# Kernel tuning notes

Measured on AMD Instinct MI355X. Metric: run time of the kernel, lower is better.

Reference implementation:

```python
import jax, jax.numpy as jnp
import numpy as np

B, C_IN, C_OUT, L = 16, 512, 512, 2048
HEADS, K, U, KS, PAD = 4, 16, 1, 3, 1
VV = C_OUT // HEADS  # 128
EPS = 1e-5


def _conv1d(x, w, pad):
    # x: [B, Cin, L], w: [Cout, Cin, KS] -> [B, Cout, L]
    return jax.lax.conv_general_dilated(
        x, w, window_strides=(1,), padding=[(pad, pad)],
        dimension_numbers=('NCH', 'OIH', 'NCH'))


def _bn_eval(y, gamma, beta, mean, var):
    # inference-mode BatchNorm1d over channel axis
    scale = gamma * jax.lax.rsqrt(var + EPS)
    shift = beta - mean * scale
    return y * scale[None, :, None] + shift[None, :, None]


def setup_inputs() -> dict:
    key = jax.random.key(0)
    ks = jax.random.split(key, 8)
    std_q = 1.0 / np.sqrt(C_IN * KS)
    x = jax.random.normal(ks[0], (B, C_IN, L), dtype=jnp.float32)
    Wq = jax.random.normal(ks[1], (K * HEADS, C_IN, KS), dtype=jnp.float32) * std_q
    Wk = jax.random.normal(ks[2], (K * U, C_IN, KS), dtype=jnp.float32) * std_q
    Wv = jax.random.normal(ks[3], (VV * U, C_IN, KS), dtype=jnp.float32) * std_q
    embedding = jax.random.normal(ks[4], (K, U), dtype=jnp.float32)
    return {
        'x': x, 'Wq': Wq,
        'q_gamma': jnp.ones((K * HEADS,), jnp.float32),
        'q_beta': jnp.zeros((K * HEADS,), jnp.float32),
        'q_mean': jnp.zeros((K * HEADS,), jnp.float32),
        'q_var': jnp.ones((K * HEADS,), jnp.float32),
        'Wk': Wk, 'Wv': Wv,
        'v_gamma': jnp.ones((VV * U,), jnp.float32),
        'v_beta': jnp.zeros((VV * U,), jnp.float32),
        'v_mean': jnp.zeros((VV * U,), jnp.float32),
        'v_var': jnp.ones((VV * U,), jnp.float32),
        'embedding': embedding,
    }


def reference(x, Wq, q_gamma, q_beta, q_mean, q_var, Wk, Wv,
              v_gamma, v_beta, v_mean, v_var, embedding):
    batch, _, n = x.shape
    # projections
    q = _bn_eval(_conv1d(x, Wq, PAD), q_gamma, q_beta, q_mean, q_var)
    q = q.reshape(batch, HEADS, K, n)                      # bhkn
    keys = _conv1d(x, Wk, PAD).reshape(batch, K, U, n)     # bkun
    sm = jax.nn.softmax(keys, axis=-1)                     # softmax over positions
    v = _bn_eval(_conv1d(x, Wv, PAD), v_gamma, v_beta, v_mean, v_var)
    v = v.reshape(batch, VV, U, n)                         # bvun
    # content lambda
    lambda_c = jnp.einsum('bkun,bvun->bkv', sm, v)
    y_c = jnp.einsum('bhkn,bkv->bhvn', q, lambda_c)
    # position lambda
    lambda_p = jnp.einsum('ku,bvun->bkvn', embedding, v)
    y_p = jnp.einsum('bhkn,bkvn->bhvn', q, lambda_p)
    out = y_c + y_p
    return out.reshape(batch, HEADS * VV, n)
```

## Files before the change

kernel.cpp:

```cpp
#include <hip/hip_runtime.h>

#define BB 16
#define CIN 512
#define LLN 2048
#define EPSV 1e-5f
#define WIMG_U16 6144

typedef __attribute__((ext_vector_type(8))) short bf16x8s;
typedef __attribute__((ext_vector_type(4))) float f32x4;

__device__ __forceinline__ unsigned short f2bf(float f) {
    union { float f; unsigned int i; } c; c.f = f;
    unsigned int x = c.i;
    unsigned int lsb = (x >> 16) & 1;
    x += 0x7fff + lsb;
    return (unsigned short)(x >> 16);
}
__device__ __forceinline__ unsigned int pack2bf(float a, float b) {
    return (unsigned int)f2bf(a) | ((unsigned int)f2bf(b) << 16);
}
__device__ __forceinline__ float bf2f(unsigned short u) {
    union { unsigned int i; float f; } c; c.i = ((unsigned int)u) << 16; return c.f;
}
__device__ __forceinline__ float bflo(unsigned int w) {
    union { unsigned int i; float f; } c; c.i = w << 16; return c.f;
}
__device__ __forceinline__ float bfhi(unsigned int w) {
    union { unsigned int i; float f; } c; c.i = w & 0xffff0000u; return c.f;
}

__device__ __forceinline__ void g2l16(const void* g, void* l) {
    typedef const __attribute__((address_space(1))) unsigned int GU;
    typedef __attribute__((address_space(3))) unsigned int LU;
    __builtin_amdgcn_global_load_lds((GU*)g, (LU*)l, 16, 0, 0);
}

__global__ __launch_bounds__(256) void prep_all(
    const float* __restrict__ x,
    const float* __restrict__ Wq, const float* __restrict__ Wk,
    const float* __restrict__ Wv,
    unsigned short* __restrict__ xpk, unsigned short* __restrict__ Wpk)
{
    const int tid = threadIdx.x;
    if (blockIdx.z < 16) {
        __shared__ __align__(16) unsigned int xs[256 * 16];
        const int nt = blockIdx.x;
        const int c  = blockIdx.y;
        const int b  = blockIdx.z;
        const int n0 = nt * 256;
        const int p  = tid >> 4;
        const int ns = (tid & 15) * 4;
        const int g = p >> 2, pi = p & 3;
        const float* x0 = x + ((size_t)b * CIN + (size_t)(c * 32 + 2 * p)) * LLN + n0;
#pragma unroll
        for (int j = 0; j < 4; j++) {
            int nl = ns + j * 64;
            float4 a = *(const float4*)&x0[nl];
            float4 bq = *(const float4*)&x0[LLN + nl];
            int rp = n0 + nl + 1;
            xs[(nl + 0) * 16 + (g ^ (((rp + 0) >> 1) & 3)) * 4 + pi] = pack2bf(a.x, bq.x);
            xs[(nl + 1) * 16 + (g ^ (((rp + 1) >> 1) & 3)) * 4 + pi] = pack2bf(a.y, bq.y);
            xs[(nl + 2) * 16 + (g ^ (((rp + 2) >> 1) & 3)) * 4 + pi] = pack2bf(a.z, bq.z);
            xs[(nl + 3) * 16 + (g ^ (((rp + 3) >> 1) & 3)) * 4 + pi] = pack2bf(a.w, bq.w);
        }
        __syncthreads();
        uint4* dst = (uint4*)(xpk + ((size_t)(b * 16 + c) * 2050 + n0 + 1) * 32);
        const uint4* srcl = (const uint4*)xs;
#pragma unroll
        for (int k = 0; k < 4; k++)
            dst[tid + k * 256] = srcl[tid + k * 256];
        if (nt == 0 && tid < 4)
            *(uint4*)(xpk + ((size_t)(b * 16 + c) * 2050) * 32 + tid * 8) = make_uint4(0, 0, 0, 0);
        if (nt == 7 && tid < 4)
            *(uint4*)(xpk + ((size_t)(b * 16 + c) * 2050 + 2049) * 32 + tid * 8) = make_uint4(0, 0, 0, 0);
    } else {
        const int wblk = blockIdx.y * 8 + blockIdx.x;
        const int img = wblk >> 1, half = wblk & 1;
        const int cot = img >> 4, chunk = img & 15;
        const int ci0 = chunk * 32;
        for (int i = half * 3072 + tid; i < half * 3072 + 3072; i += 256) {
            int t = i >> 11, r = i & 2047;
            int cf = r >> 9, lane = (r >> 3) & 63, e = i & 7;
            int lm = lane & 15, kq = lane >> 4;
            int cop = cot * 64 + cf * 16 + lm;
            int cig = ci0 + kq * 8 + e;
            float val = 0.f;
            if (cop < 64)        val = Wq[((size_t)cop * 512 + cig) * 3 + t];
            else if (cop < 80)   val = Wk[((size_t)(cop - 64) * 512 + cig) * 3 + t];
            else if (cop < 208)  val = Wv[((size_t)(cop - 80) * 512 + cig) * 3 + t];
            Wpk[(size_t)img * WIMG_U16 + i] = f2bf(val);
        }
    }
}

__global__ __launch_bounds__(512, 4) void conv_mfma(
    const unsigned short* __restrict__ xpk, const unsigned short* __restrict__ Wpk,
    const float* __restrict__ qg, const float* __restrict__ qb,
    const float* __restrict__ qm, const float* __restrict__ qv,
    const float* __restrict__ vg, const float* __restrict__ vb,
    const float* __restrict__ vm, const float* __restrict__ vvar,
    unsigned short* __restrict__ qb16, float* __restrict__ kbuf,
    unsigned short* __restrict__ vb16)
{
    __shared__ __align__(16) unsigned short xT[2][258 * 32];
    __shared__ __align__(16) unsigned short wA[2][WIMG_U16];
    __shared__ float sscale[64], sshift[64];

    const int tid = threadIdx.x;
    const int wave = tid >> 6, lane = tid & 63;
    const int kq = lane >> 4, lm = lane & 15;
    const int n0 = blockIdx.x * 256;
    const int cot = blockIdx.y;
    const int b = blockIdx.z;

    const unsigned short* xpanel = xpk + ((size_t)b * 16 * 2050 + n0) * 32;
    const unsigned short* wbase  = Wpk + (size_t)cot * 16 * WIMG_U16;

#define STAGE(buf, chunk)                                                      \
    {                                                                          \
        const unsigned short* wsrc = wbase + (size_t)(chunk) * WIMG_U16;       \
        const unsigned short* xsrc = xpanel + (size_t)(chunk) * 2050 * 32;     \
        for (int i = tid; i < 768; i += 512)  g2l16(wsrc + (size_t)i * 8, &wA[buf][i * 8]); \
        for (int i = tid; i < 1032; i += 512) g2l16(xsrc + (size_t)i * 8, &xT[buf][i * 8]); \
    }

    STAGE(0, 0)

    if (tid < 64) {
        int cop = cot * 64 + tid;
        float sc = 1.f, sh = 0.f;
        if (cop < 64) {
            float g = qg[cop], be = qb[cop], m = qm[cop], va = qv[cop];
            sc = g * rsqrtf(va + EPSV); sh = be - m * sc;
        } else if (cop >= 80 && cop < 208) {
            int cc = cop - 80;
            float g = vg[cc], be = vb[cc], m = vm[cc], va = vvar[cc];
            sc = g * rsqrtf(va + EPSV); sh = be - m * sc;
        }
        sscale[tid] = sc; sshift[tid] = sh;
    }

    f32x4 acc[4][2];
#pragma unroll
    for (int i = 0; i < 4; i++)
#pragma unroll
        for (int j = 0; j < 2; j++) acc[i][j] = (f32x4){0.f, 0.f, 0.f, 0.f};

    asm volatile("s_waitcnt vmcnt(0)" ::: "memory");
    __syncthreads();

    for (int chunk = 0; chunk < 16; chunk++) {
        const int cur = chunk & 1;
        if (chunk < 15) STAGE(cur ^ 1, chunk + 1)

#pragma unroll
        for (int t = 0; t < 3; t++) {
            bf16x8s aF[4];
#pragma unroll
            for (int cf = 0; cf < 4; cf++)
                aF[cf] = *(const bf16x8s*)&wA[cur][((t * 4 + cf) * 64 + lane) * 8];
#pragma unroll
            for (int fn = 0; fn < 2; fn++) {
                int lr = wave * 32 + fn * 16 + lm + t;
                int grp = kq ^ ((lr >> 1) & 3);
                bf16x8s bF = *(const bf16x8s*)&xT[cur][lr * 32 + grp * 8];
#pragma unroll
                for (int cf = 0; cf < 4; cf++)
                    acc[cf][fn] = __builtin_amdgcn_mfma_f32_16x16x32_bf16(
                        aF[cf], bF, acc[cf][fn], 0, 0, 0);
            }
        }
        asm volatile("s_waitcnt vmcnt(0)" ::: "memory");
        __syncthreads();
    }
#undef STAGE

#pragma unroll
    for (int cf = 0; cf < 4; cf++) {
#pragma unroll
        for (int fn = 0; fn < 2; fn++) {
#pragma unroll
            for (int r = 0; r < 4; r++) {
                int col = cf * 16 + kq * 4 + r;
                int cop = cot * 64 + col;
                if (cop >= 208) continue;
                float val = acc[cf][fn][r] * sscale[col] + sshift[col];
                int nout = n0 + wave * 32 + fn * 16 + lm;
                if (cop < 64)
                    qb16[((size_t)b * 64 + cop) * LLN + nout] = f2bf(val);
                else if (cop < 80)
                    kbuf[((size_t)b * 16 + (cop - 64)) * LLN + nout] = __expf(val - 16.f);
                else
                    vb16[((size_t)b * 128 + (cop - 80)) * LLN + nout] = f2bf(val);
            }
        }
    }
}

__global__ __launch_bounds__(256) void lambdac_kernel(
    const float* __restrict__ kexp, const unsigned short* __restrict__ vb16,
    float* __restrict__ lc2, float* __restrict__ s2)
{
    const int wave = threadIdx.x >> 6;
    const int lane = threadIdx.x & 63;
    const int idx = blockIdx.x;
    const int half = idx & 1;
    const int vgp = (idx >> 1) & 31;
    const int b = idx >> 6;
    const float* ps = kexp + ((size_t)b * 16 + wave * 4) * LLN + half * 1024;
    const unsigned short* pv = vb16 + ((size_t)b * 128 + vgp * 4) * LLN + half * 1024;

    float sum[4] = {0.f, 0.f, 0.f, 0.f};
    float acc[4][4];
#pragma unroll
    for (int k = 0; k < 4; k++)
#pragma unroll
        for (int v = 0; v < 4; v++) acc[k][v] = 0.f;
#pragma unroll
    for (int j = 0; j < 2; j++) {
        int n = (j * 64 + lane) * 8;
        float e[4][8];
#pragma unroll
        for (int k = 0; k < 4; k++) {
            float4 a = *(const float4*)&ps[(size_t)k * LLN + n];
            float4 c = *(const float4*)&ps[(size_t)k * LLN + n + 4];
            e[k][0] = a.x; e[k][1] = a.y; e[k][2] = a.z; e[k][3] = a.w;
            e[k][4] = c.x; e[k][5] = c.y; e[k][6] = c.z; e[k][7] = c.w;
            sum[k] += a.x + a.y + a.z + a.w + c.x + c.y + c.z + c.w;
        }
#pragma unroll
        for (int v = 0; v < 4; v++) {
            uint4 w = *(const uint4*)&pv[(size_t)v * LLN + n];
            float vv[8] = {bflo(w.x), bfhi(w.x), bflo(w.y), bfhi(w.y),
                           bflo(w.z), bfhi(w.z), bflo(w.w), bfhi(w.w)};
#pragma unroll
            for (int k = 0; k < 4; k++) {
                float t = 0.f;
#pragma unroll
                for (int q = 0; q < 8; q++) t += e[k][q] * vv[q];
                acc[k][v] += t;
            }
        }
    }
#pragma unroll
    for (int k = 0; k < 4; k++) {
#pragma unroll
        for (int off = 32; off > 0; off >>= 1)
            sum[k] += __shfl_xor(sum[k], off, 64);
#pragma unroll
        for (int v = 0; v < 4; v++)
#pragma unroll
            for (int off = 32; off > 0; off >>= 1)
                acc[k][v] += __shfl_xor(acc[k][v], off, 64);
    }
    if (lane == 0) {
#pragma unroll
        for (int k = 0; k < 4; k++) {
#pragma unroll
            for (int v = 0; v < 4; v++)
                lc2[(((size_t)half * 16 + b) * 16 + wave * 4 + k) * 128 + vgp * 4 + v]
                    = acc[k][v];
            if (vgp == 0)
                s2[((size_t)half * 16 + b) * 16 + wave * 4 + k] = sum[k];
        }
    }
}

__global__ __launch_bounds__(256) void final_kernel(
    const unsigned short* __restrict__ qb16, const unsigned short* __restrict__ vb16,
    const float* __restrict__ lc2, const float* __restrict__ s2,
    const float* __restrict__ emb, float* __restrict__ out)
{
    __shared__ float lcsT[64][16];
    __shared__ float es[16], invd[16];
    const int tid = threadIdx.x;
    const int h = tid >> 6, nl = tid & 63;
    const int n0 = blockIdx.x * 64;
    const int vh = blockIdx.y * 64;
    const int b = blockIdx.z;

    if (tid < 16) {
        es[tid] = emb[tid];
        invd[tid] = 1.f / (s2[(size_t)b * 16 + tid] + s2[256 + (size_t)b * 16 + tid]);
    }
    __syncthreads();
    for (int i = tid; i < 1024; i += 256) {
        int k = i & 15, vl = i >> 4;
        float l0 = lc2[((size_t)b * 16 + k) * 128 + vh + vl];
        float l1 = lc2[(size_t)32768 + ((size_t)b * 16 + k) * 128 + vh + vl];
        lcsT[vl][k] = (l0 + l1) * invd[k];
    }
    __syncthreads();

    const int n = n0 + nl;
    const unsigned short* pq = qb16 + ((size_t)b * 64 + h * 16) * LLN + n;
    float4 q4[4];
#pragma unroll
    for (int kk = 0; kk < 4; kk++) {
        q4[kk].x = bf2f(pq[(size_t)(kk * 4 + 0) * LLN]);
        q4[kk].y = bf2f(pq[(size_t)(kk * 4 + 1) * LLN]);
        q4[kk].z = bf2f(pq[(size_t)(kk * 4 + 2) * LLN]);
        q4[kk].w = bf2f(pq[(size_t)(kk * 4 + 3) * LLN]);
    }
    float s = 0.f;
#pragma unroll
    for (int kk = 0; kk < 4; kk++)
        s += q4[kk].x * es[kk * 4] + q4[kk].y * es[kk * 4 + 1]
           + q4[kk].z * es[kk * 4 + 2] + q4[kk].w * es[kk * 4 + 3];

    const unsigned short* pv = vb16 + ((size_t)b * 128 + vh) * LLN + n;
    float* po = out + ((size_t)b * 512 + h * 128 + vh) * LLN + n;
#pragma unroll 4
    for (int v = 0; v < 64; v++) {
        const float* lrow = &lcsT[v][0];
        float4 c0 = *(const float4*)&lrow[0];
        float4 c1 = *(const float4*)&lrow[4];
        float4 c2 = *(const float4*)&lrow[8];
        float4 c3 = *(const float4*)&lrow[12];
        float lam = q4[0].x * c0.x + q4[0].y * c0.y + q4[0].z * c0.z + q4[0].w * c0.w
                  + q4[1].x * c1.x + q4[1].y * c1.y + q4[1].z * c1.z + q4[1].w * c1.w
                  + q4[2].x * c2.x + q4[2].y * c2.y + q4[2].z * c2.z + q4[2].w * c2.w
                  + q4[3].x * c3.x + q4[3].y * c3.y + q4[3].z * c3.z + q4[3].w * c3.w;
        float vvv = bf2f(pv[(size_t)v * LLN]);
        po[(size_t)v * LLN] = lam + s * vvv;
    }
}

extern "C" void kernel_launch(void* const* d_in, const int* in_sizes, int n_in,
                              void* d_out, int out_size, void* d_ws, size_t ws_size,
                              hipStream_t stream)
{
    const float* x   = (const float*)d_in[0];
    const float* Wq  = (const float*)d_in[1];
    const float* qg  = (const float*)d_in[2];
    const float* qb  = (const float*)d_in[3];
    const float* qm  = (const float*)d_in[4];
    const float* qv  = (const float*)d_in[5];
    const float* Wk  = (const float*)d_in[6];
    const float* Wv  = (const float*)d_in[7];
    const float* vg  = (const float*)d_in[8];
    const float* vb  = (const float*)d_in[9];
    const float* vm  = (const float*)d_in[10];
    const float* vva = (const float*)d_in[11];
    const float* emb = (const float*)d_in[12];
    float* out = (float*)d_out;

    float* kbuf = (float*)d_ws;
    float* lc2  = kbuf + (size_t)BB * 16 * LLN;
    float* s2   = lc2 + (size_t)2 * BB * 16 * 128;
    unsigned short* qb16 = (unsigned short*)(s2 + 512);
    unsigned short* vb16 = qb16 + (size_t)BB * 64 * LLN;
    unsigned short* Wpk  = vb16 + (size_t)BB * 128 * LLN;
    unsigned short* xpk  = Wpk + (size_t)64 * WIMG_U16;

    hipLaunchKernelGGL(prep_all, dim3(8, 16, 17), dim3(256), 0, stream,
                       x, Wq, Wk, Wv, xpk, Wpk);

    hipLaunchKernelGGL(conv_mfma, dim3(8, 4, 16), dim3(512), 0, stream,
                       xpk, Wpk, qg, qb, qm, qv, vg, vb, vm, vva,
                       qb16, kbuf, vb16);

    hipLaunchKernelGGL(lambdac_kernel, dim3(1024), dim3(256), 0, stream,
                       kbuf, vb16, lc2, s2);

    hipLaunchKernelGGL(final_kernel, dim3(32, 2, BB), dim3(256), 0, stream,
                       qb16, vb16, lc2, s2, emb, out);
}
```

Before: 190.8 us.

## Fuse x bf16 packing into conv kernel, loading fp32 x directly into LDS

Removes the separate x pre-pack pass (fp32 to bf16 transposed panel in global memory). The conv kernel now streams fp32 x tiles into LDS asynchronously, loads halo columns separately, and transposes and converts to bf16 in LDS before each chunk's MFMA work. The goal is to avoid writing and re-reading an intermediate packed x buffer. In exchange, the 4 cot blocks each re-read fp32 x (twice the bytes of bf16). Each chunk also gains an extra barrier and transpose step, and the larger LDS footprint may reduce occupancy.

```diff
diff --git a/kernel.cpp b/kernel.cpp
--- a/kernel.cpp
+++ b/kernel.cpp
@@ -1,4 +1,5 @@
 #include <hip/hip_runtime.h>
+#include <hip/hip_bf16.h>
 
 #define BB 16
 #define CIN 512
@@ -16,9 +17,6 @@
     x += 0x7fff + lsb;
     return (unsigned short)(x >> 16);
 }
-__device__ __forceinline__ unsigned int pack2bf(float a, float b) {
-    return (unsigned int)f2bf(a) | ((unsigned int)f2bf(b) << 16);
-}
 __device__ __forceinline__ float bf2f(unsigned short u) {
     union { unsigned int i; float f; } c; c.i = ((unsigned int)u) << 16; return c.f;
 }
@@ -27,6 +25,11 @@
 }
 __device__ __forceinline__ float bfhi(unsigned int w) {
     union { unsigned int i; float f; } c; c.i = w & 0xffff0000u; return c.f;
+}
+__device__ __forceinline__ unsigned int cvtpk2(float a, float b) {
+    union { __hip_bfloat162 h; unsigned int u; } c;
+    c.h = __float22bfloat162_rn(float2{a, b});
+    return c.u;
 }
 
 __device__ __forceinline__ void g2l16(const void* g, void* l) {
@@ -35,66 +38,31 @@
     __builtin_amdgcn_global_load_lds((GU*)g, (LU*)l, 16, 0, 0);
 }
 
-__global__ __launch_bounds__(256) void prep_all(
-    const float* __restrict__ x,
+__global__ __launch_bounds__(256) void prep_w(
     const float* __restrict__ Wq, const float* __restrict__ Wk,
-    const float* __restrict__ Wv,
-    unsigned short* __restrict__ xpk, unsigned short* __restrict__ Wpk)
+    const float* __restrict__ Wv, unsigned short* __restrict__ Wpk)
 {
     const int tid = threadIdx.x;
-    if (blockIdx.z < 16) {
-        __shared__ __align__(16) unsigned int xs[256 * 16];
-        const int nt = blockIdx.x;
-        const int c  = blockIdx.y;
-        const int b  = blockIdx.z;
-        const int n0 = nt * 256;
-        const int p  = tid >> 4;
-        const int ns = (tid & 15) * 4;
-        const int g = p >> 2, pi = p & 3;
-        const float* x0 = x + ((size_t)b * CIN + (size_t)(c * 32 + 2 * p)) * LLN + n0;
-#pragma unroll
-        for (int j = 0; j < 4; j++) {
-            int nl = ns + j * 64;
-            float4 a = *(const float4*)&x0[nl];
-            float4 bq = *(const float4*)&x0[LLN + nl];
-            int rp = n0 + nl + 1;
-            xs[(nl + 0) * 16 + (g ^ (((rp + 0) >> 1) & 3)) * 4 + pi] = pack2bf(a.x, bq.x);
-            xs[(nl + 1) * 16 + (g ^ (((rp + 1) >> 1) & 3)) * 4 + pi] = pack2bf(a.y, bq.y);
-            xs[(nl + 2) * 16 + (g ^ (((rp + 2) >> 1) & 3)) * 4 + pi] = pack2bf(a.z, bq.z);
-            xs[(nl + 3) * 16 + (g ^ (((rp + 3) >> 1) & 3)) * 4 + pi] = pack2bf(a.w, bq.w);
-        }
-        __syncthreads();
-        uint4* dst = (uint4*)(xpk + ((size_t)(b * 16 + c) * 2050 + n0 + 1) * 32);
-        const uint4* srcl = (const uint4*)xs;
-#pragma unroll
-        for (int k = 0; k < 4; k++)
-            dst[tid + k * 256] = srcl[tid + k * 256];
-        if (nt == 0 && tid < 4)
-            *(uint4*)(xpk + ((size_t)(b * 16 + c) * 2050) * 32 + tid * 8) = make_uint4(0, 0, 0, 0);
-        if (nt == 7 && tid < 4)
-            *(uint4*)(xpk + ((size_t)(b * 16 + c) * 2050 + 2049) * 32 + tid * 8) = make_uint4(0, 0, 0, 0);
-    } else {
-        const int wblk = blockIdx.y * 8 + blockIdx.x;
-        const int img = wblk >> 1, half = wblk & 1;
-        const int cot = img >> 4, chunk = img & 15;
-        const int ci0 = chunk * 32;
-        for (int i = half * 3072 + tid; i < half * 3072 + 3072; i += 256) {
-            int t = i >> 11, r = i & 2047;
-            int cf = r >> 9, lane = (r >> 3) & 63, e = i & 7;
-            int lm = lane & 15, kq = lane >> 4;
-            int cop = cot * 64 + cf * 16 + lm;
-            int cig = ci0 + kq * 8 + e;
-            float val = 0.f;
-            if (cop < 64)        val = Wq[((size_t)cop * 512 + cig) * 3 + t];
-            else if (cop < 80)   val = Wk[((size_t)(cop - 64) * 512 + cig) * 3 + t];
-            else if (cop < 208)  val = Wv[((size_t)(cop - 80) * 512 + cig) * 3 + t];
-            Wpk[(size_t)img * WIMG_U16 + i] = f2bf(val);
-        }
+    const int wblk = blockIdx.y * 8 + blockIdx.x;
+    const int img = wblk >> 1, half = wblk & 1;
+    const int cot = img >> 4, chunk = img & 15;
+    const int ci0 = chunk * 32;
+    for (int i = half * 3072 + tid; i < half * 3072 + 3072; i += 256) {
+        int t = i >> 11, r = i & 2047;
+        int cf = r >> 9, lane = (r >> 3) & 63, e = i & 7;
+        int lm = lane & 15, kq = lane >> 4;
+        int cop = cot * 64 + cf * 16 + lm;
+        int cig = ci0 + kq * 8 + e;
+        float val = 0.f;
+        if (cop < 64)        val = Wq[((size_t)cop * 512 + cig) * 3 + t];
+        else if (cop < 80)   val = Wk[((size_t)(cop - 64) * 512 + cig) * 3 + t];
+        else if (cop < 208)  val = Wv[((size_t)(cop - 80) * 512 + cig) * 3 + t];
+        Wpk[(size_t)img * WIMG_U16 + i] = f2bf(val);
     }
 }
 
 __global__ __launch_bounds__(512, 4) void conv_mfma(
-    const unsigned short* __restrict__ xpk, const unsigned short* __restrict__ Wpk,
+    const float* __restrict__ x, const unsigned short* __restrict__ Wpk,
     const float* __restrict__ qg, const float* __restrict__ qb,
     const float* __restrict__ qm, const float* __restrict__ qv,
     const float* __restrict__ vg, const float* __restrict__ vb,
@@ -102,8 +70,9 @@
     unsigned short* __restrict__ qb16, float* __restrict__ kbuf,
     unsigned short* __restrict__ vb16)
 {
-    __shared__ __align__(16) unsigned short xT[2][258 * 32];
+    __shared__ __align__(16) unsigned short xT[258 * 32];
     __shared__ __align__(16) unsigned short wA[2][WIMG_U16];
+    __shared__ __align__(16) float xs32[32 * 256];
     __shared__ float sscale[64], sshift[64];
 
     const int tid = threadIdx.x;
@@ -113,18 +82,65 @@
     const int cot = blockIdx.y;
     const int b = blockIdx.z;
 
-    const unsigned short* xpanel = xpk + ((size_t)b * 16 * 2050 + n0) * 32;
-    const unsigned short* wbase  = Wpk + (size_t)cot * 16 * WIMG_U16;
-
-#define STAGE(buf, chunk)                                                      \
-    {                                                                          \
-        const unsigned short* wsrc = wbase + (size_t)(chunk) * WIMG_U16;       \
-        const unsigned short* xsrc = xpanel + (size_t)(chunk) * 2050 * 32;     \
-        for (int i = tid; i < 768; i += 512)  g2l16(wsrc + (size_t)i * 8, &wA[buf][i * 8]); \
-        for (int i = tid; i < 1032; i += 512) g2l16(xsrc + (size_t)i * 8, &xT[buf][i * 8]); \
-    }
-
-    STAGE(0, 0)
+    const float* xb = x + (size_t)b * CIN * LLN;
+    const unsigned short* wbase = Wpk + (size_t)cot * 16 * WIMG_U16;
+
+    float hl0 = 0.f, hl1 = 0.f;
+
+#define STAGE_X32(chunk)                                                        \
+    {                                                                           \
+        const float* src = xb + (size_t)(chunk) * 32 * LLN + n0;                \
+        _Pragma("unroll")                                                       \
+        for (int j = 0; j < 4; j++) {                                           \
+            int i = tid + j * 512;                                              \
+            g2l16(src + (size_t)(i >> 6) * LLN + (i & 63) * 4,                  \
+                  (char*)xs32 + (size_t)i * 16);                                \
+        }                                                                       \
+    }
+#define STAGE_W(buf, chunk)                                                     \
+    {                                                                           \
+        const unsigned short* wsrc = wbase + (size_t)(chunk) * WIMG_U16;        \
+        for (int i = tid; i < 768; i += 512)                                    \
+            g2l16(wsrc + (size_t)i * 8, &wA[buf][i * 8]);                       \
+    }
+#define HALO_ISSUE(chunk)                                                       \
+    if (tid < 32) {                                                             \
+        int side = tid & 1, p = tid >> 1;                                       \
+        int nh = side ? (n0 + 256) : (n0 - 1);                                  \
+        hl0 = 0.f; hl1 = 0.f;                                                   \
+        if (nh >= 0 && nh < LLN) {                                              \
+            hl0 = xb[((size_t)(chunk) * 32 + 2 * p) * LLN + nh];                \
+            hl1 = xb[((size_t)(chunk) * 32 + 2 * p + 1) * LLN + nh];            \
+        }                                                                       \
+    }
+#define TRANSPOSE()                                                             \
+    {                                                                           \
+        int nl = tid >> 1, h = tid & 1, rp = nl + 1;                            \
+        int sig = (rp >> 1) & 3;                                                \
+        unsigned short* row = &xT[rp * 32];                                     \
+        _Pragma("unroll")                                                       \
+        for (int g2 = 0; g2 < 2; g2++) {                                        \
+            int gg = h * 2 + g2;                                                \
+            float f0 = xs32[(gg * 8 + 0) * 256 + nl];                           \
+            float f1 = xs32[(gg * 8 + 1) * 256 + nl];                           \
+            float f2 = xs32[(gg * 8 + 2) * 256 + nl];                           \
+            float f3 = xs32[(gg * 8 + 3) * 256 + nl];                           \
+            float f4 = xs32[(gg * 8 + 4) * 256 + nl];                           \
+            float f5 = xs32[(gg * 8 + 5) * 256 + nl];                           \
+            float f6 = xs32[(gg * 8 + 6) * 256 + nl];                           \
+            float f7 = xs32[(gg * 8 + 7) * 256 + nl];                           \
+            uint4 w = make_uint4(cvtpk2(f0, f1), cvtpk2(f2, f3),                \
+                                 cvtpk2(f4, f5), cvtpk2(f6, f7));               \
+            *(uint4*)&row[(gg ^ sig) * 8] = w;                                  \
+        }                                                                       \
+        if (tid < 32) {                                                         \
+            int side = tid & 1, p = tid >> 1;                                   \
+            int hr = side ? 257 : 0;             \
+            *(unsigned int*)&xT[hr * 32 + p * 2] = cvtpk2(hl0, hl1);            \
+        }                                                                       \
+    }
+
+    STAGE_X32(0) STAGE_W(0, 0) HALO_ISSUE(0)
 
     if (tid < 64) {
         int cop = cot * 64 + tid;
@@ -148,10 +164,12 @@
 
     asm volatile("s_waitcnt vmcnt(0)" ::: "memory");
     __syncthreads();
+    TRANSPOSE()
+    __syncthreads();
 
     for (int chunk = 0; chunk < 16; chunk++) {
         const int cur = chunk & 1;
-        if (chunk < 15) STAGE(cur ^ 1, chunk + 1)
+        if (chunk < 15) { STAGE_X32(chunk + 1) STAGE_W(cur ^ 1, chunk + 1) HALO_ISSUE(chunk + 1) }
 
 #pragma unroll
         for (int t = 0; t < 3; t++) {
@@ -163,7 +181,7 @@
             for (int fn = 0; fn < 2; fn++) {
                 int lr = wave * 32 + fn * 16 + lm + t;
                 int grp = kq ^ ((lr >> 1) & 3);
-                bf16x8s bF = *(const bf16x8s*)&xT[cur][lr * 32 + grp * 8];
+                bf16x8s bF = *(const bf16x8s*)&xT[lr * 32 + grp * 8];
 #pragma unroll
                 for (int cf = 0; cf < 4; cf++)
                     acc[cf][fn] = __builtin_amdgcn_mfma_f32_16x16x32_bf16(
@@ -172,8 +190,12 @@
         }
         asm volatile("s_waitcnt vmcnt(0)" ::: "memory");
         __syncthreads();
-    }
-#undef STAGE
+        if (chunk < 15) { TRANSPOSE() __syncthreads(); }
+    }
+#undef STAGE_X32
+#undef STAGE_W
+#undef HALO_ISSUE
+#undef TRANSPOSE
 
 #pragma unroll
     for (int cf = 0; cf < 4; cf++) {
@@ -351,13 +373,11 @@
     unsigned short* qb16 = (unsigned short*)(s2 + 512);
     unsigned short* vb16 = qb16 + (size_t)BB * 64 * LLN;
     unsigned short* Wpk  = vb16 + (size_t)BB * 128 * LLN;
-    unsigned short* xpk  = Wpk + (size_t)64 * WIMG_U16;
-
-    hipLaunchKernelGGL(prep_all, dim3(8, 16, 17), dim3(256), 0, stream,
-                       x, Wq, Wk, Wv, xpk, Wpk);
+
+    hipLaunchKernelGGL(prep_w, dim3(8, 16), dim3(256), 0, stream, Wq, Wk, Wv, Wpk);
 
     hipLaunchKernelGGL(conv_mfma, dim3(8, 4, 16), dim3(512), 0, stream,
-                       xpk, Wpk, qg, qb, qm, qv, vg, vb, vm, vva,
+                       x, Wpk, qg, qb, qm, qv, vg, vb, vm, vva,
                        qb16, kbuf, vb16);
 
     hipLaunchKernelGGL(lambdac_kernel, dim3(1024), dim3(256), 0, stream,
```

After: 190.2 us. Within noise of the previous version (-0.3%).
